# Kernel optimization log

Measured on AMD Instinct MI355X. Metric: run time of the kernel, lower is better.

## Reference

```python
import jax, jax.numpy as jnp
import numpy as np

B, N, D, H = 8, 2048, 512, 512


def setup_inputs() -> dict:
    key = jax.random.key(0)
    kx, kwq, kbq, kwk, kbk = jax.random.split(key, 5)
    s = 1.0 / np.sqrt(D)
    return {
        "x": jax.random.normal(kx, (B, N, D), dtype=jnp.float32),
        "Wq": jax.random.uniform(kwq, (D, H), jnp.float32, -s, s),
        "bq": jax.random.uniform(kbq, (H,), jnp.float32, -s, s),
        "Wk": jax.random.uniform(kwk, (D, H), jnp.float32, -s, s),
        "bk": jax.random.uniform(kbk, (H,), jnp.float32, -s, s),
    }


def reference(x, Wq, bq, Wk, bk):
    # x: [B, N, D]
    q = jnp.einsum("bnd,dh->bnh", x, Wq) + bq          # [B, N, H]
    k = jnp.einsum("bnd,dh->bnh", x, Wk) + bk          # [B, N, H]
    energy = jnp.einsum("bih,bjh->bij", q, k)           # [B, N, N] (no scaling)
    # NOTE: softmax over dim=1 (the QUERY axis), not the usual key axis.
    attn = jax.nn.softmax(energy, axis=1)               # [B, N, N]
    out = jnp.einsum("bij,bjd->bid", attn, x)           # V = x
    return out
```

## Files before the change

### kernel.cpp

```cpp
#include <hip/hip_runtime.h>
#include <hip/hip_bf16.h>
#include <cstdio>

typedef float f32x4 __attribute__((ext_vector_type(4)));
typedef __bf16 bf16x8 __attribute__((ext_vector_type(8)));

static constexpr int Bn = 8, Nn = 2048, Dn = 512, Hn = 512;

__device__ __forceinline__ unsigned short f2bf(float x) {
    union { float f; unsigned int u; } v; v.f = x;
    unsigned int r = (v.u + 0x7FFFu + ((v.u >> 16) & 1u)) >> 16;
    return (unsigned short)r;
}
__device__ __forceinline__ float bf2f(unsigned short h) {
    union { unsigned int u; float f; } v; v.u = ((unsigned int)h) << 16;
    return v.f;
}

__device__ __forceinline__ void gload_lds16(const unsigned short* g, unsigned short* l) {
    __builtin_amdgcn_global_load_lds(
        (const __attribute__((address_space(1))) void*)g,
        (__attribute__((address_space(3))) void*)l,
        16, 0, 0);
}

__device__ __forceinline__ int xcd_swizzle(int lin, int nwg) {
    return (lin & 7) * (nwg >> 3) + (lin >> 3);
}

__global__ void cast_x_kernel(const float* __restrict__ x, unsigned short* __restrict__ xb, int n) {
    int i = (blockIdx.x * blockDim.x + threadIdx.x) * 8;
    if (i >= n) return;
    float4 a = *(const float4*)(x + i);
    float4 b = *(const float4*)(x + i + 4);
    unsigned short tmp[8] = {f2bf(a.x), f2bf(a.y), f2bf(a.z), f2bf(a.w),
                             f2bf(b.x), f2bf(b.y), f2bf(b.z), f2bf(b.w)};
    *(uint4*)(xb + i) = *(const uint4*)tmp;
}

__global__ __launch_bounds__(256) void transpose_cast_kernel(
    const float* __restrict__ in, unsigned short* __restrict__ out,
    const float* __restrict__ sdiv, int R, int C)
{
    __shared__ float tile[64][65];
    const int z = blockIdx.z;
    const float* inb = in + (size_t)z * R * C;
    unsigned short* outb = out + (size_t)z * R * C;
    const int r0 = blockIdx.y * 64, c0 = blockIdx.x * 64;
    const int tx = threadIdx.x & 63, ty = threadIdx.x >> 6;
#pragma unroll
    for (int p = 0; p < 64; p += 4) {
        const int r = p + ty;
        float v = inb[(size_t)(r0 + r) * C + c0 + tx];
        if (sdiv) v /= sdiv[(size_t)z * R + r0 + r];
        tile[r][tx] = v;
    }
    __syncthreads();
#pragma unroll
    for (int p = 0; p < 64; p += 4) {
        const int oc = p + ty;
        outb[(size_t)(c0 + oc) * R + r0 + tx] = f2bf(tile[tx][oc]);
    }
}

__global__ void combine_s_kernel(const float* __restrict__ s_part, float* __restrict__ s,
                                 int nblk, int total) {
    int i = blockIdx.x * blockDim.x + threadIdx.x;
    if (i >= total) return;
    int z = i >> 11, j = i & (Nn - 1);
    float acc = 0.f;
    for (int p = 0; p < nblk; ++p) acc += s_part[((size_t)z * nblk + p) * Nn + j];
    s[i] = acc;
}

template<int MODE>
__global__ __launch_bounds__(256, 2) void gemm_bt(
    const unsigned short* __restrict__ A, long long sA, int lda,
    const unsigned short* __restrict__ Bt, long long sB, int ldb,
    void* __restrict__ Cp, long long sC,
    const float* __restrict__ bias, const float* __restrict__ bias2, int bsplit,
    float* __restrict__ s_part,
    int M, int N, int K, int gx, int gy)
{
    __shared__ unsigned short As[128 * 64];
    __shared__ unsigned short Bs[128 * 64];
    __shared__ float s_red[256];

    const int lin = xcd_swizzle(blockIdx.x, gridDim.x);
    const int bz = lin / (gx * gy);
    const int rem = lin - bz * gx * gy;
    const int by = rem / gx;
    const int bx = rem - by * gx;

    const unsigned short* Ab = A + (size_t)bz * sA;
    const unsigned short* Bb = Bt + (size_t)bz * sB;
    const int i0 = by * 128, j0 = bx * 128;

    const int t = threadIdx.x;
    const int lane = t & 63;
    const int wave = t >> 6;
    const int wr = wave >> 1, wc = wave & 1;
    const int l15 = lane & 15, g = lane >> 4;

    f32x4 acc[4][4];
    const f32x4 zero4 = {0.f, 0.f, 0.f, 0.f};
#pragma unroll
    for (int mi = 0; mi < 4; ++mi)
#pragma unroll
        for (int ni = 0; ni < 4; ++ni) acc[mi][ni] = zero4;

    const int rbase = wave * 32;
    const int lrow = lane >> 3;
    const int gch = (lane & 7) ^ lrow;

    for (int kt = 0; kt < K; kt += 64) {
#pragma unroll
        for (int i = 0; i < 4; ++i) {
            const int r = rbase + i * 8 + lrow;
            gload_lds16(Ab + (size_t)(i0 + r) * lda + kt + gch * 8, As + (rbase + i * 8) * 64);
            gload_lds16(Bb + (size_t)(j0 + r) * ldb + kt + gch * 8, Bs + (rbase + i * 8) * 64);
        }
        __syncthreads();
#pragma unroll
        for (int kk = 0; kk < 64; kk += 32) {
            const int sl0 = (kk >> 3) + g;
            bf16x8 af[4], bfr[4];
#pragma unroll
            for (int mi = 0; mi < 4; ++mi) {
                const int row = wr * 64 + mi * 16 + l15;
                af[mi] = *(const bf16x8*)(As + row * 64 + ((sl0 ^ (row & 7)) * 8));
            }
#pragma unroll
            for (int ni = 0; ni < 4; ++ni) {
                const int row = wc * 64 + ni * 16 + l15;
                bfr[ni] = *(const bf16x8*)(Bs + row * 64 + ((sl0 ^ (row & 7)) * 8));
            }
#pragma unroll
            for (int mi = 0; mi < 4; ++mi)
#pragma unroll
                for (int ni = 0; ni < 4; ++ni)
                    acc[mi][ni] = __builtin_amdgcn_mfma_f32_16x16x32_bf16(af[mi], bfr[ni], acc[mi][ni], 0, 0, 0);
        }
        __syncthreads();
    }

    if (MODE == 0) {
        unsigned short* C = (unsigned short*)Cp;
#pragma unroll
        for (int ni = 0; ni < 4; ++ni) {
            const int col = j0 + wc * 64 + ni * 16 + l15;
            const float bv = (col < bsplit) ? bias[col] : bias2[col - bsplit];
#pragma unroll
            for (int mi = 0; mi < 4; ++mi) {
                const int rb = i0 + wr * 64 + mi * 16 + g * 4;
#pragma unroll
                for (int r = 0; r < 4; ++r)
                    C[(size_t)(rb + r) * N + col] = f2bf(acc[mi][ni][r] + bv);
            }
        }
    } else if (MODE == 1) {
        unsigned short* C = (unsigned short*)Cp + (size_t)bz * sC;
        float cs[4] = {0.f, 0.f, 0.f, 0.f};
#pragma unroll
        for (int ni = 0; ni < 4; ++ni) {
            const int col = j0 + wc * 64 + ni * 16 + l15;
#pragma unroll
            for (int mi = 0; mi < 4; ++mi) {
                const int rb = i0 + wr * 64 + mi * 16 + g * 4;
#pragma unroll
                for (int r = 0; r < 4; ++r) {
                    const float e = __expf(acc[mi][ni][r]);
                    const unsigned short h = f2bf(e);
                    C[(size_t)(rb + r) * N + col] = h;
                    cs[ni] += bf2f(h);
                }
            }
        }
#pragma unroll
        for (int ni = 0; ni < 4; ++ni) {
            cs[ni] += __shfl_xor(cs[ni], 16);
            cs[ni] += __shfl_xor(cs[ni], 32);
        }
        if (g == 0) {
#pragma unroll
            for (int ni = 0; ni < 4; ++ni)
                s_red[wr * 128 + wc * 64 + ni * 16 + l15] = cs[ni];
        }
        __syncthreads();
        if (t < 128) {
            const float sp = s_red[t] + s_red[128 + t];
            s_part[((size_t)bz * gy + by) * N + j0 + t] = sp;
        }
    } else {
        float* C = (float*)Cp + (size_t)bz * sC;
#pragma unroll
        for (int ni = 0; ni < 4; ++ni) {
            const int col = j0 + wc * 64 + ni * 16 + l15;
#pragma unroll
            for (int mi = 0; mi < 4; ++mi) {
                const int rb = i0 + wr * 64 + mi * 16 + g * 4;
#pragma unroll
                for (int r = 0; r < 4; ++r)
                    C[(size_t)(rb + r) * N + col] = acc[mi][ni][r];
            }
        }
    }
}

extern "C" void kernel_launch(void* const* d_in, const int* in_sizes, int n_in,
                              void* d_out, int out_size, void* d_ws, size_t ws_size,
                              hipStream_t stream) {
    const float* x  = (const float*)d_in[0];
    const float* Wq = (const float*)d_in[1];
    const float* bq = (const float*)d_in[2];
    const float* Wk = (const float*)d_in[3];
    const float* bk = (const float*)d_in[4];
    float* out = (float*)d_out;

    char* ws = (char*)d_ws;
    unsigned short* xb    = (unsigned short*)(ws);
    unsigned short* qk    = (unsigned short*)(ws + (16ull << 20));
    unsigned short* WqkT  = (unsigned short*)(ws + (48ull << 20));
    unsigned short* xsT   = (unsigned short*)(ws + (49ull << 20));
    float*          s_prt = (float*)(ws + (65ull << 20));
    float*          s     = (float*)(ws + (66ull << 20));
    unsigned short* expE  = (unsigned short*)(ws + (67ull << 20));
    if (ws_size < (131ull << 20)) {
        fprintf(stderr, "WS TOO SMALL: have %zu need %llu\n", ws_size, (131ull << 20));
    }

    cast_x_kernel<<<dim3((Bn * Nn * Dn) / (8 * 256)), 256, 0, stream>>>(x, xb, Bn * Nn * Dn);
    transpose_cast_kernel<<<dim3(Hn / 64, Dn / 64, 1), 256, 0, stream>>>(Wq, WqkT, nullptr, Dn, Hn);
    transpose_cast_kernel<<<dim3(Hn / 64, Dn / 64, 1), 256, 0, stream>>>(Wk, WqkT + (size_t)Hn * Dn, nullptr, Dn, Hn);
    {
        const int gx = (2 * Hn) / 128, gy = (Bn * Nn) / 128;
        gemm_bt<0><<<dim3(gx * gy), 256, 0, stream>>>(
            xb, 0, Dn, WqkT, 0, Dn, qk, 0, bq, bk, Hn, nullptr,
            Bn * Nn, 2 * Hn, Dn, gx, gy);
    }
    {
        const int gx = Nn / 128, gy = Nn / 128;
        gemm_bt<1><<<dim3(gx * gy * Bn), 256, 0, stream>>>(
            qk, (long long)Nn * 2 * Hn, 2 * Hn,
            qk + Hn, (long long)Nn * 2 * Hn, 2 * Hn,
            expE, (long long)Nn * Nn, nullptr, nullptr, 0, s_prt,
            Nn, Nn, Hn, gx, gy);
    }
    combine_s_kernel<<<dim3((Bn * Nn) / 256), 256, 0, stream>>>(s_prt, s, Nn / 128, Bn * Nn);
    transpose_cast_kernel<<<dim3(Dn / 64, Nn / 64, Bn), 256, 0, stream>>>(x, xsT, s, Nn, Dn);
    {
        const int gx = Dn / 128, gy = Nn / 128;
        gemm_bt<2><<<dim3(gx * gy * Bn), 256, 0, stream>>>(
            expE, (long long)Nn * Nn, Nn, xsT, (long long)Dn * Nn, Nn,
            out, (long long)Nn * Dn, nullptr, nullptr, 0, nullptr,
            Nn, Dn, Nn, gx, gy);
    }
}
```

Before: 145.5 us.

## Double-buffer GEMM LDS, switch to 32x32 MFMA, and cut prep-kernel traffic

The GEMM kernel now double-buffers its LDS tiles so the next K-tile's global-to-LDS loads overlap the current tile's MFMAs. It also switches from 16x16x32 to 32x32x16 bf16 MFMA with a new fragment layout and raises wave priority around the MFMA block. Separately, the two weight transpose launches are merged into one, and the scaled x transpose now reads the bf16 copy of x instead of fp32. The workspace is compacted by reusing the qk region for xsT. This doubles LDS use per block, which may limit occupancy, and scaling from bf16 x adds a second rounding step.

Result: slower. 159.3 us (+9.5%).

```diff
diff --git a/kernel.cpp b/kernel.cpp
--- a/kernel.cpp
+++ b/kernel.cpp
@@ -3,6 +3,7 @@
 #include <cstdio>
 
 typedef float f32x4 __attribute__((ext_vector_type(4)));
+typedef float f32x16 __attribute__((ext_vector_type(16)));
 typedef __bf16 bf16x8 __attribute__((ext_vector_type(8)));
 
 static constexpr int Bn = 8, Nn = 2048, Dn = 512, Hn = 512;
@@ -38,28 +39,50 @@
     *(uint4*)(xb + i) = *(const uint4*)tmp;
 }
 
-__global__ __launch_bounds__(256) void transpose_cast_kernel(
-    const float* __restrict__ in, unsigned short* __restrict__ out,
-    const float* __restrict__ sdiv, int R, int C)
+__global__ __launch_bounds__(256) void transpose_cast_w(
+    const float* __restrict__ Wq, const float* __restrict__ Wk,
+    unsigned short* __restrict__ out)
 {
     __shared__ float tile[64][65];
     const int z = blockIdx.z;
-    const float* inb = in + (size_t)z * R * C;
-    unsigned short* outb = out + (size_t)z * R * C;
+    const float* inb = z ? Wk : Wq;
+    unsigned short* outb = out + (size_t)z * Hn * Dn;
     const int r0 = blockIdx.y * 64, c0 = blockIdx.x * 64;
     const int tx = threadIdx.x & 63, ty = threadIdx.x >> 6;
 #pragma unroll
     for (int p = 0; p < 64; p += 4) {
         const int r = p + ty;
-        float v = inb[(size_t)(r0 + r) * C + c0 + tx];
-        if (sdiv) v /= sdiv[(size_t)z * R + r0 + r];
-        tile[r][tx] = v;
+        tile[r][tx] = inb[(size_t)(r0 + r) * Hn + c0 + tx];
     }
     __syncthreads();
 #pragma unroll
     for (int p = 0; p < 64; p += 4) {
         const int oc = p + ty;
-        outb[(size_t)(c0 + oc) * R + r0 + tx] = f2bf(tile[tx][oc]);
+        outb[(size_t)(c0 + oc) * Dn + r0 + tx] = f2bf(tile[tx][oc]);
+    }
+}
+
+__global__ __launch_bounds__(256) void transpose_scale_bf16(
+    const unsigned short* __restrict__ xb, unsigned short* __restrict__ out,
+    const float* __restrict__ s)
+{
+    __shared__ unsigned short tile[64][65];
+    const int z = blockIdx.z;
+    const unsigned short* inb = xb + (size_t)z * Nn * Dn;
+    unsigned short* ob = out + (size_t)z * Nn * Dn;
+    const int j0 = blockIdx.y * 64, d0 = blockIdx.x * 64;
+    const int tx = threadIdx.x & 63, ty = threadIdx.x >> 6;
+#pragma unroll
+    for (int p = 0; p < 64; p += 4) {
+        const int r = p + ty;
+        tile[r][tx] = inb[(size_t)(j0 + r) * Dn + d0 + tx];
+    }
+    __syncthreads();
+    const float sv = s[(size_t)z * Nn + j0 + tx];
+#pragma unroll
+    for (int p = 0; p < 64; p += 4) {
+        const int oc = p + ty;
+        ob[(size_t)(d0 + oc) * Nn + j0 + tx] = f2bf(bf2f(tile[tx][oc]) / sv);
     }
 }
 
@@ -74,7 +97,7 @@
 }
 
 template<int MODE>
-__global__ __launch_bounds__(256, 2) void gemm_bt(
+__global__ __launch_bounds__(256, 2) void gemd(
     const unsigned short* __restrict__ A, long long sA, int lda,
     const unsigned short* __restrict__ Bt, long long sB, int ldb,
     void* __restrict__ Cp, long long sC,
@@ -82,9 +105,8 @@
     float* __restrict__ s_part,
     int M, int N, int K, int gx, int gy)
 {
-    __shared__ unsigned short As[128 * 64];
-    __shared__ unsigned short Bs[128 * 64];
-    __shared__ float s_red[256];
+    __shared__ unsigned short As[2][128 * 64];
+    __shared__ unsigned short Bs[2][128 * 64];
 
     const int lin = xcd_swizzle(blockIdx.x, gridDim.x);
     const int bz = lin / (gx * gy);
@@ -99,111 +121,125 @@
     const int t = threadIdx.x;
     const int lane = t & 63;
     const int wave = t >> 6;
-    const int wr = wave >> 1, wc = wave & 1;
-    const int l15 = lane & 15, g = lane >> 4;
-
-    f32x4 acc[4][4];
-    const f32x4 zero4 = {0.f, 0.f, 0.f, 0.f};
-#pragma unroll
-    for (int mi = 0; mi < 4; ++mi)
-#pragma unroll
-        for (int ni = 0; ni < 4; ++ni) acc[mi][ni] = zero4;
+    const int wm = wave >> 1, wn = wave & 1;
+    const int r5 = lane & 31, h = lane >> 5;
+
+    const int arow = (wm * 64 + r5) * 128;
+    const int brow = (wn * 64 + r5) * 128;
+    int csw[4];
+#pragma unroll
+    for (int kq = 0; kq < 4; ++kq) csw[kq] = ((kq * 2 + h) ^ (r5 & 7)) * 16;
+
+    f32x16 acc[2][2];
+#pragma unroll
+    for (int af = 0; af < 2; ++af)
+#pragma unroll
+        for (int bf = 0; bf < 2; ++bf)
+#pragma unroll
+            for (int r = 0; r < 16; ++r) acc[af][bf][r] = 0.f;
 
     const int rbase = wave * 32;
     const int lrow = lane >> 3;
     const int gch = (lane & 7) ^ lrow;
 
-    for (int kt = 0; kt < K; kt += 64) {
-#pragma unroll
-        for (int i = 0; i < 4; ++i) {
-            const int r = rbase + i * 8 + lrow;
-            gload_lds16(Ab + (size_t)(i0 + r) * lda + kt + gch * 8, As + (rbase + i * 8) * 64);
-            gload_lds16(Bb + (size_t)(j0 + r) * ldb + kt + gch * 8, Bs + (rbase + i * 8) * 64);
+#define STAGE(s, ktv)                                                          \
+    {                                                                          \
+        _Pragma("unroll")                                                      \
+        for (int i = 0; i < 4; ++i) {                                          \
+            const int r = rbase + i * 8 + lrow;                                \
+            gload_lds16(Ab + (size_t)(i0 + r) * lda + (ktv) + gch * 8,         \
+                        &As[s][(rbase + i * 8) * 64]);                         \
+            gload_lds16(Bb + (size_t)(j0 + r) * ldb + (ktv) + gch * 8,         \
+                        &Bs[s][(rbase + i * 8) * 64]);                         \
+        }                                                                      \
+    }
+
+    STAGE(0, 0);
+    asm volatile("s_waitcnt vmcnt(0)" ::: "memory");
+    asm volatile("s_barrier" ::: "memory");
+
+    const int NT = K >> 6;
+    for (int T = 0; T < NT; ++T) {
+        const int cur = T & 1;
+        if (T + 1 < NT) STAGE(cur ^ 1, (T + 1) * 64);
+#pragma unroll
+        for (int kq = 0; kq < 4; ++kq) {
+            bf16x8 a0 = *(const bf16x8*)((const char*)&As[cur][0] + arow + csw[kq]);
+            bf16x8 a1 = *(const bf16x8*)((const char*)&As[cur][0] + arow + 4096 + csw[kq]);
+            bf16x8 b0 = *(const bf16x8*)((const char*)&Bs[cur][0] + brow + csw[kq]);
+            bf16x8 b1 = *(const bf16x8*)((const char*)&Bs[cur][0] + brow + 4096 + csw[kq]);
+            __builtin_amdgcn_s_setprio(1);
+            acc[0][0] = __builtin_amdgcn_mfma_f32_32x32x16_bf16(a0, b0, acc[0][0], 0, 0, 0);
+            acc[0][1] = __builtin_amdgcn_mfma_f32_32x32x16_bf16(a0, b1, acc[0][1], 0, 0, 0);
+            acc[1][0] = __builtin_amdgcn_mfma_f32_32x32x16_bf16(a1, b0, acc[1][0], 0, 0, 0);
+            acc[1][1] = __builtin_amdgcn_mfma_f32_32x32x16_bf16(a1, b1, acc[1][1], 0, 0, 0);
+            __builtin_amdgcn_s_setprio(0);
+        }
+        asm volatile("s_waitcnt vmcnt(0)" ::: "memory");
+        asm volatile("s_barrier" ::: "memory");
+    }
+#undef STAGE
+
+    const int col0 = j0 + wn * 64 + r5;
+    if (MODE == 0) {
+        unsigned short* C = (unsigned short*)Cp;
+        float bv[2];
+#pragma unroll
+        for (int bf = 0; bf < 2; ++bf) {
+            const int col = col0 + bf * 32;
+            bv[bf] = (col < bsplit) ? bias[col] : bias2[col - bsplit];
+        }
+#pragma unroll
+        for (int af = 0; af < 2; ++af)
+#pragma unroll
+            for (int reg = 0; reg < 16; ++reg) {
+                const int row = i0 + wm * 64 + af * 32 + (reg & 3) + 8 * (reg >> 2) + 4 * h;
+                unsigned short* Crow = C + (size_t)row * N + col0;
+#pragma unroll
+                for (int bf = 0; bf < 2; ++bf)
+                    Crow[bf * 32] = f2bf(acc[af][bf][reg] + bv[bf]);
+            }
+    } else if (MODE == 1) {
+        unsigned short* C = (unsigned short*)Cp + (size_t)bz * sC;
+        float cs[2] = {0.f, 0.f};
+#pragma unroll
+        for (int af = 0; af < 2; ++af)
+#pragma unroll
+            for (int reg = 0; reg < 16; ++reg) {
+                const int row = i0 + wm * 64 + af * 32 + (reg & 3) + 8 * (reg >> 2) + 4 * h;
+                unsigned short* Crow = C + (size_t)row * N + col0;
+#pragma unroll
+                for (int bf = 0; bf < 2; ++bf) {
+                    const float e = __expf(acc[af][bf][reg]);
+                    const unsigned short hh = f2bf(e);
+                    Crow[bf * 32] = hh;
+                    cs[bf] += bf2f(hh);
+                }
+            }
+#pragma unroll
+        for (int bf = 0; bf < 2; ++bf) cs[bf] += __shfl_xor(cs[bf], 32);
+        __syncthreads();
+        float* red = (float*)&As[0][0];
+        if (h == 0) {
+#pragma unroll
+            for (int bf = 0; bf < 2; ++bf)
+                red[wm * 128 + wn * 64 + bf * 32 + r5] = cs[bf];
         }
         __syncthreads();
-#pragma unroll
-        for (int kk = 0; kk < 64; kk += 32) {
-            const int sl0 = (kk >> 3) + g;
-            bf16x8 af[4], bfr[4];
-#pragma unroll
-            for (int mi = 0; mi < 4; ++mi) {
-                const int row = wr * 64 + mi * 16 + l15;
-                af[mi] = *(const bf16x8*)(As + row * 64 + ((sl0 ^ (row & 7)) * 8));
-            }
-#pragma unroll
-            for (int ni = 0; ni < 4; ++ni) {
-                const int row = wc * 64 + ni * 16 + l15;
-                bfr[ni] = *(const bf16x8*)(Bs + row * 64 + ((sl0 ^ (row & 7)) * 8));
-            }
-#pragma unroll
-            for (int mi = 0; mi < 4; ++mi)
-#pragma unroll
-                for (int ni = 0; ni < 4; ++ni)
-                    acc[mi][ni] = __builtin_amdgcn_mfma_f32_16x16x32_bf16(af[mi], bfr[ni], acc[mi][ni], 0, 0, 0);
-        }
-        __syncthreads();
-    }
-
-    if (MODE == 0) {
-        unsigned short* C = (unsigned short*)Cp;
-#pragma unroll
-        for (int ni = 0; ni < 4; ++ni) {
-            const int col = j0 + wc * 64 + ni * 16 + l15;
-            const float bv = (col < bsplit) ? bias[col] : bias2[col - bsplit];
-#pragma unroll
-            for (int mi = 0; mi < 4; ++mi) {
-                const int rb = i0 + wr * 64 + mi * 16 + g * 4;
-#pragma unroll
-                for (int r = 0; r < 4; ++r)
-                    C[(size_t)(rb + r) * N + col] = f2bf(acc[mi][ni][r] + bv);
-            }
-        }
-    } else if (MODE == 1) {
-        unsigned short* C = (unsigned short*)Cp + (size_t)bz * sC;
-        float cs[4] = {0.f, 0.f, 0.f, 0.f};
-#pragma unroll
-        for (int ni = 0; ni < 4; ++ni) {
-            const int col = j0 + wc * 64 + ni * 16 + l15;
-#pragma unroll
-            for (int mi = 0; mi < 4; ++mi) {
-                const int rb = i0 + wr * 64 + mi * 16 + g * 4;
-#pragma unroll
-                for (int r = 0; r < 4; ++r) {
-                    const float e = __expf(acc[mi][ni][r]);
-                    const unsigned short h = f2bf(e);
-                    C[(size_t)(rb + r) * N + col] = h;
-                    cs[ni] += bf2f(h);
-                }
-            }
-        }
-#pragma unroll
-        for (int ni = 0; ni < 4; ++ni) {
-            cs[ni] += __shfl_xor(cs[ni], 16);
-            cs[ni] += __shfl_xor(cs[ni], 32);
-        }
-        if (g == 0) {
-#pragma unroll
-            for (int ni = 0; ni < 4; ++ni)
-                s_red[wr * 128 + wc * 64 + ni * 16 + l15] = cs[ni];
-        }
-        __syncthreads();
-        if (t < 128) {
-            const float sp = s_red[t] + s_red[128 + t];
-            s_part[((size_t)bz * gy + by) * N + j0 + t] = sp;
-        }
+        if (t < 128)
+            s_part[((size_t)bz * gy + by) * Nn + j0 + t] = red[t] + red[128 + t];
     } else {
         float* C = (float*)Cp + (size_t)bz * sC;
 #pragma unroll
-        for (int ni = 0; ni < 4; ++ni) {
-            const int col = j0 + wc * 64 + ni * 16 + l15;
-#pragma unroll
-            for (int mi = 0; mi < 4; ++mi) {
-                const int rb = i0 + wr * 64 + mi * 16 + g * 4;
-#pragma unroll
-                for (int r = 0; r < 4; ++r)
-                    C[(size_t)(rb + r) * N + col] = acc[mi][ni][r];
+        for (int af = 0; af < 2; ++af)
+#pragma unroll
+            for (int reg = 0; reg < 16; ++reg) {
+                const int row = i0 + wm * 64 + af * 32 + (reg & 3) + 8 * (reg >> 2) + 4 * h;
+                float* Crow = C + (size_t)row * N + col0;
+#pragma unroll
+                for (int bf = 0; bf < 2; ++bf)
+                    Crow[bf * 32] = acc[af][bf][reg];
             }
-        }
     }
 }
 
@@ -220,37 +256,36 @@
     char* ws = (char*)d_ws;
     unsigned short* xb    = (unsigned short*)(ws);
     unsigned short* qk    = (unsigned short*)(ws + (16ull << 20));
+    unsigned short* xsT   = (unsigned short*)(ws + (16ull << 20));
     unsigned short* WqkT  = (unsigned short*)(ws + (48ull << 20));
-    unsigned short* xsT   = (unsigned short*)(ws + (49ull << 20));
-    float*          s_prt = (float*)(ws + (65ull << 20));
-    float*          s     = (float*)(ws + (66ull << 20));
-    unsigned short* expE  = (unsigned short*)(ws + (67ull << 20));
-    if (ws_size < (131ull << 20)) {
-        fprintf(stderr, "WS TOO SMALL: have %zu need %llu\n", ws_size, (131ull << 20));
+    float*          s_prt = (float*)(ws + (49ull << 20));
+    float*          s     = (float*)(ws + (51ull << 20));
+    unsigned short* expE  = (unsigned short*)(ws + (52ull << 20));
+    if (ws_size < (116ull << 20)) {
+        fprintf(stderr, "WS TOO SMALL: have %zu need %llu\n", ws_size, (116ull << 20));
     }
 
     cast_x_kernel<<<dim3((Bn * Nn * Dn) / (8 * 256)), 256, 0, stream>>>(x, xb, Bn * Nn * Dn);
-    transpose_cast_kernel<<<dim3(Hn / 64, Dn / 64, 1), 256, 0, stream>>>(Wq, WqkT, nullptr, Dn, Hn);
-    transpose_cast_kernel<<<dim3(Hn / 64, Dn / 64, 1), 256, 0, stream>>>(Wk, WqkT + (size_t)Hn * Dn, nullptr, Dn, Hn);
+    transpose_cast_w<<<dim3(Hn / 64, Dn / 64, 2), 256, 0, stream>>>(Wq, Wk, WqkT);
     {
         const int gx = (2 * Hn) / 128, gy = (Bn * Nn) / 128;
-        gemm_bt<0><<<dim3(gx * gy), 256, 0, stream>>>(
+        gemd<0><<<dim3(gx * gy), 256, 0, stream>>>(
             xb, 0, Dn, WqkT, 0, Dn, qk, 0, bq, bk, Hn, nullptr,
             Bn * Nn, 2 * Hn, Dn, gx, gy);
     }
     {
         const int gx = Nn / 128, gy = Nn / 128;
-        gemm_bt<1><<<dim3(gx * gy * Bn), 256, 0, stream>>>(
+        gemd<1><<<dim3(gx * gy * Bn), 256, 0, stream>>>(
             qk, (long long)Nn * 2 * Hn, 2 * Hn,
             qk + Hn, (long long)Nn * 2 * Hn, 2 * Hn,
             expE, (long long)Nn * Nn, nullptr, nullptr, 0, s_prt,
             Nn, Nn, Hn, gx, gy);
     }
     combine_s_kernel<<<dim3((Bn * Nn) / 256), 256, 0, stream>>>(s_prt, s, Nn / 128, Bn * Nn);
-    transpose_cast_kernel<<<dim3(Dn / 64, Nn / 64, Bn), 256, 0, stream>>>(x, xsT, s, Nn, Dn);
+    transpose_scale_bf16<<<dim3(Dn / 64, Nn / 64, Bn), 256, 0, stream>>>(xb, xsT, s);
     {
         const int gx = Dn / 128, gy = Nn / 128;
-        gemm_bt<2><<<dim3(gx * gy * Bn), 256, 0, stream>>>(
+        gemd<2><<<dim3(gx * gy * Bn), 256, 0, stream>>>(
             expE, (long long)Nn * Nn, Nn, xsT, (long long)Dn * Nn, Nn,
             out, (long long)Nn * Dn, nullptr, nullptr, 0, nullptr,
             Nn, Dn, Nn, gx, gy);
```
